# Performance work log

Hardware: AMD Instinct MI355X
Metric: run time of the kernel (lower is better)

The kernel has to match this reference:

```python
import jax, jax.numpy as jnp
import numpy as np

B, S, D, H = 8, 2048, 256, 4
HD = D // H  # 64
EPS = 1e-5


def setup_inputs() -> dict:
    key = jax.random.key(0)
    ks = jax.random.split(key, 16)
    sc = 0.05
    return {
        "descriptors": jax.random.normal(ks[0], (B, S, D), jnp.float32),
        "source": jax.random.normal(ks[1], (B, S, D), jnp.float32),
        "mask": jnp.ones((B, S), jnp.int32),
        # attention projections (stored as [in, out])
        "q_w": jax.random.normal(ks[2], (D, D), jnp.float32) * sc,
        "q_b": jnp.zeros((D,), jnp.float32),
        "k_w": jax.random.normal(ks[3], (D, D), jnp.float32) * sc,
        "k_b": jnp.zeros((D,), jnp.float32),
        "v_w": jax.random.normal(ks[4], (D, D), jnp.float32) * sc,
        "v_b": jnp.zeros((D,), jnp.float32),
        "o_w": jax.random.normal(ks[5], (D, D), jnp.float32) * sc,
        "o_b": jnp.zeros((D,), jnp.float32),
        # MLP layer 0: 2D -> 2D, BatchNorm1d (eval mode) + ReLU
        "m0_w": jax.random.normal(ks[6], (2 * D, 2 * D), jnp.float32) * sc,
        "m0_b": jnp.zeros((2 * D,), jnp.float32),
        "bn_g": jax.random.uniform(ks[7], (2 * D,), jnp.float32, 0.5, 1.5),
        "bn_b": jax.random.normal(ks[8], (2 * D,), jnp.float32) * 0.1,
        "bn_m": jax.random.normal(ks[9], (2 * D,), jnp.float32) * 0.1,
        "bn_v": jax.random.uniform(ks[10], (2 * D,), jnp.float32, 0.5, 1.5),
        # MLP layer 1: 2D -> D, no activation
        "m1_w": jax.random.normal(ks[11], (2 * D, D), jnp.float32) * sc,
        "m1_b": jnp.zeros((D,), jnp.float32),
    }


def reference(descriptors, source, mask, q_w, q_b, k_w, k_b, v_w, v_b, o_w, o_b,
              m0_w, m0_b, bn_g, bn_b, bn_m, bn_v, m1_w, m1_b):
    # Multi-head cross-attention: query=descriptors, key=value=source
    q = (descriptors @ q_w + q_b).reshape(B, S, H, HD).transpose(0, 2, 1, 3)  # [B,H,S,HD]
    k = (source @ k_w + k_b).reshape(B, S, H, HD).transpose(0, 2, 1, 3)
    v = (source @ v_w + v_b).reshape(B, S, H, HD).transpose(0, 2, 1, 3)

    scores = jnp.einsum("bhqd,bhkd->bhqk", q, k) / jnp.sqrt(jnp.float32(HD))
    scores = jnp.where(mask[:, None, None, :] == 0, -1e9, scores)
    probs = jax.nn.softmax(scores.astype(jnp.float32), axis=-1)  # [B,H,S,S]

    ctx = jnp.einsum("bhqk,bhkd->bhqd", probs, v)  # [B,H,S,HD]
    ctx = ctx.transpose(0, 2, 1, 3).reshape(B, S, D)
    attn_out = ctx @ o_w + o_b  # out_proj

    # concat + MLP (Linear -> BatchNorm1d(eval) -> ReLU -> Linear)
    h = jnp.concatenate([descriptors, attn_out], axis=-1)  # [B,S,2D]
    h = h @ m0_w + m0_b
    h = (h - bn_m) * jax.lax.rsqrt(bn_v + EPS) * bn_g + bn_b  # per-channel BN
    h = jax.nn.relu(h)
    h = h @ m1_w + m1_b  # [B,S,D]
    return h
```

## Files before the change

kernel.cpp:

```cpp
#include <hip/hip_runtime.h>

#define NB 8
#define NS 2048
#define ND 256
#define NH 4
#define NHD 64
#define ND2 512
#define NM (NB * NS)
#define C1 0.18033688f

typedef __attribute__((ext_vector_type(8))) short          bf16x8;
typedef __attribute__((ext_vector_type(4))) float          f32x4;
typedef __attribute__((ext_vector_type(16))) float         f32x16;
typedef unsigned short ushort_t;
typedef unsigned int   uint_t;

#define MFMA16(a, b, c) __builtin_amdgcn_mfma_f32_16x16x32_bf16(a, b, c, 0, 0, 0)
#define MFMA32(a, b, c) __builtin_amdgcn_mfma_f32_32x32x16_bf16(a, b, c, 0, 0, 0)

#if __has_builtin(__builtin_amdgcn_exp2f)
#define EXP2(x) __builtin_amdgcn_exp2f(x)
#else
#define EXP2(x) exp2f(x)
#endif

static __device__ inline uint_t pack2bf(float a, float b) {
    union { float f; uint_t u; } x, y; x.f = a; y.f = b;
    return __builtin_amdgcn_perm(y.u + 0x8000u, x.u + 0x8000u, 0x07060302u);
}
static __device__ inline ushort_t f2bf(float f) {
    union { float f; uint_t u; } x; x.f = f;
    return (ushort_t)((x.u + 0x7FFFu + ((x.u >> 16) & 1u)) >> 16);
}
static __device__ inline uint_t cvtpk_bf16(float a, float b) {
    uint_t r;
    asm("v_cvt_pk_bf16_f32 %0, %1, %2" : "=v"(r) : "v"(a), "v"(b));
    return r;
}
static __device__ inline void plswap(uint_t &a, uint_t &b) {
    asm("v_permlane32_swap_b32 %0, %1" : "+v"(a), "+v"(b));
}


static __device__ inline void femit(ushort_t* buf, int n, int k, float v) {
    const int kc = k >> 5;
    const int lane = (((k >> 3) & 3) << 4) | (n & 15);
    const int j = k & 7;
    buf[((size_t)(((n >> 4) * 16 + kc) * 64 + lane)) * 8 + j] = f2bf(v);
}

__global__ __launch_bounds__(256) void prep(
    const float* __restrict__ desc, const float* __restrict__ srcp,
    const int* __restrict__ mask,
    const float* __restrict__ q_w, const float* __restrict__ k_w,
    const float* __restrict__ v_w, const float* __restrict__ m1_w,
    const float* __restrict__ o_w, const float* __restrict__ o_b,
    const float* __restrict__ m0_w, const float* __restrict__ m0_b,
    const float* __restrict__ bng, const float* __restrict__ bnb,
    const float* __restrict__ bnm, const float* __restrict__ bnv,
    ushort_t* __restrict__ descF, ushort_t* __restrict__ srcF,
    ushort_t* __restrict__ qwF, ushort_t* __restrict__ kwF,
    ushort_t* __restrict__ vwF, ushort_t* __restrict__ m1F,
    ushort_t* __restrict__ m0fF, float* __restrict__ biasf,
    uint_t* __restrict__ mbits)
{
    __shared__ float ow[256];
    const int blk = blockIdx.x;
    const int t = threadIdx.x;

    if (blk < 4096) {
        const int y = blk >> 11, x = blk & 2047;
        const float* src = y ? srcp : desc;
        ushort_t* dst    = y ? srcF : descF;
        const int g = x * 256 + t;
        const int lane = g & 63, ci = g >> 6;
        const int kc = ci & 7, r16 = ci >> 3;
        const int row = r16 * 16 + (lane & 15);
        const int c0  = kc * 32 + (lane >> 4) * 8;
        const float* p = src + (size_t)row * ND + c0;
        float4 a = *(const float4*)p;
        float4 b = *(const float4*)(p + 4);
        uint4 pk;
        pk.x = pack2bf(a.x, a.y); pk.y = pack2bf(a.z, a.w);
        pk.z = pack2bf(b.x, b.y); pk.w = pack2bf(b.z, b.w);
        *(uint4*)(dst + (size_t)g * 8) = pk;
    } else if (blk < 4352) {
        const int wb = blk - 4096;
        const int y = wb >> 6, x = wb & 63;
        const float* src; ushort_t* dst; int K, N; float sc = 1.0f;
        switch (y) {
            case 0: src = q_w; dst = qwF; K = 256; N = 256; sc = C1; break;
            case 1: src = k_w; dst = kwF; K = 256; N = 256; break;
            case 2: src = v_w; dst = vwF; K = 256; N = 256; break;
            default: src = m1_w; dst = m1F; K = 512; N = 256; break;
        }
        const int g = x * 256 + t;
        if (g >= (N * K) / 8) return;
        const int lane = g & 63, ci = g >> 6;
        const int lgck = (K == 512) ? 4 : 3;
        const int kc = ci & ((1 << lgck) - 1), n16 = ci >> lgck;
        const int n  = n16 * 16 + (lane & 15);
        const int k0 = kc * 32 + (lane >> 4) * 8;
        float f[8];
#pragma unroll
        for (int j = 0; j < 8; j++) f[j] = src[(size_t)(k0 + j) * N + n] * sc;
        uint4 pk;
        pk.x = pack2bf(f[0], f[1]); pk.y = pack2bf(f[2], f[3]);
        pk.z = pack2bf(f[4], f[5]); pk.w = pack2bf(f[6], f[7]);
        *(uint4*)(dst + (size_t)g * 8) = pk;
    } else if (blk < 4354) {
        const int g = (blk - 4352) * 256 + t;
        const int base = g * 32;
        uint_t m = 0;
#pragma unroll
        for (int j = 0; j < 32; j++) m |= (mask[base + j] ? 1u : 0u) << j;
        mbits[g] = m;
    } else if (blk < 4610) {
        const int i = blk - 4354;
        ow[t] = o_w[i * 256 + t];
        __syncthreads();
        float f0 = 0.f, f1 = 0.f;
#pragma unroll 4
        for (int j = 0; j < 256; j++) {
            const float w = ow[j];
            f0 += w * m0_w[(size_t)(256 + j) * 512 + t];
            f1 += w * m0_w[(size_t)(256 + j) * 512 + t + 256];
        }
        const float A0v = bng[t] * rsqrtf(bnv[t] + 1e-5f);
        const float A1v = bng[t + 256] * rsqrtf(bnv[t + 256] + 1e-5f);
        femit(m0fF, t, 256 + i, f0 * A0v);
        femit(m0fF, t + 256, 256 + i, f1 * A1v);
        femit(m0fF, t, i, m0_w[(size_t)i * 512 + t] * A0v);
        femit(m0fF, t + 256, i, m0_w[(size_t)i * 512 + t + 256] * A1v);
    } else {
        const int bb = blk - 4610;
        const int n  = bb * 32 + (t >> 3);
        const int jp = t & 7;
        float s = 0.f;
#pragma unroll 4
        for (int j = jp * 32; j < jp * 32 + 32; j++)
            s += o_b[j] * m0_w[(size_t)(256 + j) * 512 + n];
        s += __shfl_xor(s, 1);
        s += __shfl_xor(s, 2);
        s += __shfl_xor(s, 4);
        if (jp == 0) {
            const float A = bng[n] * rsqrtf(bnv[n] + 1e-5f);
            biasf[n] = (m0_b[n] + s - bnm[n]) * A + bnb[n];
        }
    }
}

template <int KC, int AK, bool NAT, int MT>
static __device__ inline void core(
    const ushort_t* __restrict__ A0, const ushort_t* __restrict__ A1,
    const ushort_t* __restrict__ WF, int t16, int n16, f32x4 acc[MT][4])
{
    const int lane = threadIdx.x & 63;
#pragma unroll
    for (int kc = 0; kc < KC; kc++) {
        const ushort_t* Ab = (kc < AK) ? A0 : A1;
        const int kca = (kc < AK) ? kc : kc - AK;
        bf16x8 af[MT], wf[4];
#pragma unroll
        for (int mt = 0; mt < MT; mt++)
            af[mt] = *(const bf16x8*)(Ab + ((size_t)((t16 + mt) * AK + kca) * 64 + lane) * 8);
#pragma unroll
        for (int nt = 0; nt < 4; nt++)
            wf[nt] = *(const bf16x8*)(WF + ((size_t)((n16 + nt) * KC + kc) * 64 + lane) * 8);
#pragma unroll
        for (int mt = 0; mt < MT; mt++)
#pragma unroll
            for (int nt = 0; nt < 4; nt++) {
                if (NAT) acc[mt][nt] = MFMA16(af[mt], wf[nt], acc[mt][nt]);
                else     acc[mt][nt] = MFMA16(wf[nt], af[mt], acc[mt][nt]);
            }
    }
}

__global__ __launch_bounds__(256) void qkv_frag(
    const ushort_t* __restrict__ descF, const ushort_t* __restrict__ srcF,
    const ushort_t* __restrict__ qwF, const ushort_t* __restrict__ kwF,
    const ushort_t* __restrict__ vwF,
    const float* __restrict__ q_b, const float* __restrict__ k_b,
    const float* __restrict__ v_b,
    ushort_t* __restrict__ qF, ushort_t* __restrict__ kF,
    ushort_t* __restrict__ vF)
{
    const int t = threadIdx.x, w = t >> 6;
    const int lq = t & 15, lg = (t & 63) >> 4;
    const int h    = blockIdx.x;
    const int tok0 = (blockIdx.y << 7) + (w << 5);
    const int t16  = tok0 >> 4, n16 = h << 2;
    const int z    = blockIdx.z;

    f32x4 acc[2][4];
#pragma unroll
    for (int mt = 0; mt < 2; mt++)
#pragma unroll
        for (int nt = 0; nt < 4; nt++) acc[mt][nt] = (f32x4){0.f, 0.f, 0.f, 0.f};

    if (z == 2) {
        core<8, 8, true, 2>(srcF, srcF, vwF, t16, n16, acc);
#pragma unroll
        for (int nt = 0; nt < 4; nt++) {
            const int dvh = nt * 16 + lq;
            const float bs = v_b[h * 64 + dvh];
#pragma unroll
            for (int mt = 0; mt < 2; mt++) {
                const int tok = tok0 + mt * 16 + lg * 4;
                const int b = tok >> 11, s0 = tok & 2047;
                const int bh = b * NH + h;
                uint2 pv;
                pv.x = pack2bf(acc[mt][nt][0] + bs, acc[mt][nt][1] + bs);
                pv.y = pack2bf(acc[mt][nt][2] + bs, acc[mt][nt][3] + bs);
                const size_t e = (size_t)bh * 131072 +
                    ((size_t)((dvh >> 4) * 64 + (s0 >> 5)) * 64 +
                     (((s0 >> 3) & 3) * 16 + (dvh & 15))) * 8 + (s0 & 7);
                *(uint2*)(vF + e) = pv;
            }
        }
    } else {
        const ushort_t* A = z ? srcF : descF;
        const ushort_t* W = z ? kwF : qwF;
        const float* bias = z ? k_b : q_b;
        ushort_t* dst     = z ? kF : qF;
        const float bsc   = z ? 1.0f : C1;
        core<8, 8, false, 2>(A, A, W, t16, n16, acc);
#pragma unroll
        for (int nt = 0; nt < 4; nt++) {
            const int d0 = nt * 16 + lg * 4;
            f32x4 b4 = *(const f32x4*)(bias + h * 64 + d0);
#pragma unroll
            for (int mt = 0; mt < 2; mt++) {
                const int tok = tok0 + mt * 16 + lq;
                const int b = tok >> 11, s = tok & 2047;
                const int bh = b * NH + h;
                uint2 pv;
                pv.x = pack2bf(acc[mt][nt][0] + b4[0] * bsc,
                               acc[mt][nt][1] + b4[1] * bsc);
                pv.y = pack2bf(acc[mt][nt][2] + b4[2] * bsc,
                               acc[mt][nt][3] + b4[3] * bsc);
                const size_t e = (size_t)bh * 131072 +
                    ((size_t)((s >> 4) * 2 + (d0 >> 5)) * 64 +
                     (((d0 >> 3) & 3) * 16 + lq)) * 8 + (d0 & 7);
                *(uint2*)(dst + e) = pv;
            }
        }
    }
}

__global__ __launch_bounds__(256) void mlp0_frag(
    const ushort_t* __restrict__ descF, const ushort_t* __restrict__ ctxF,
    const ushort_t* __restrict__ m0fF, const float* __restrict__ biasf,
    ushort_t* __restrict__ hF)
{
    const int t = threadIdx.x, w = t >> 6;
    const int lq = t & 15, lg = (t & 63) >> 4;
    const int n0   = blockIdx.x << 6;
    const int tok0 = (blockIdx.y << 7) + (w << 5);
    const int t16  = tok0 >> 4, n16 = n0 >> 4;

    f32x4 acc[2][4];
#pragma unroll
    for (int mt = 0; mt < 2; mt++)
#pragma unroll
        for (int nt = 0; nt < 4; nt++) acc[mt][nt] = (f32x4){0.f, 0.f, 0.f, 0.f};

    core<16, 8, false, 2>(descF, ctxF, m0fF, t16, n16, acc);

#pragma unroll
    for (int nt = 0; nt < 4; nt++) {
        const int c0 = n0 + nt * 16 + lg * 4;
        f32x4 b4 = *(const f32x4*)(biasf + c0);
#pragma unroll
        for (int mt = 0; mt < 2; mt++) {
            const int tok = tok0 + mt * 16 + lq;
            uint2 pv;
            pv.x = pack2bf(fmaxf(acc[mt][nt][0] + b4[0], 0.f),
                           fmaxf(acc[mt][nt][1] + b4[1], 0.f));
            pv.y = pack2bf(fmaxf(acc[mt][nt][2] + b4[2], 0.f),
                           fmaxf(acc[mt][nt][3] + b4[3], 0.f));
            const size_t e = ((size_t)((tok >> 4) * 16 + (c0 >> 5)) * 64 +
                              (((c0 >> 3) & 3) * 16 + lq)) * 8 + (c0 & 7);
            *(uint2*)(hF + e) = pv;
        }
    }
}

__global__ __launch_bounds__(256) void mlp1_frag(
    const ushort_t* __restrict__ hF, const ushort_t* __restrict__ m1F,
    const float* __restrict__ m1_b, float* __restrict__ out)
{
    const int t = threadIdx.x, w = t >> 6;
    const int lq = t & 15, lg = (t & 63) >> 4;
    const int n0   = blockIdx.x << 6;
    const int tok0 = (blockIdx.y << 6) + (w << 4);
    const int t16  = tok0 >> 4, n16 = n0 >> 4;

    f32x4 acc[1][4];
#pragma unroll
    for (int nt = 0; nt < 4; nt++) acc[0][nt] = (f32x4){0.f, 0.f, 0.f, 0.f};

    core<16, 16, false, 1>(hF, hF, m1F, t16, n16, acc);

#pragma unroll
    for (int nt = 0; nt < 4; nt++) {
        const int c0 = n0 + nt * 16 + lg * 4;
        f32x4 b4 = *(const f32x4*)(m1_b + c0);
        const int tok = tok0 + lq;
        f32x4 o4;
#pragma unroll
        for (int j = 0; j < 4; j++) o4[j] = acc[0][nt][j] + b4[j];
        *(f32x4*)(out + (size_t)tok * ND + c0) = o4;
    }
}

__global__ __launch_bounds__(256) void attn_frag(
    const ushort_t* __restrict__ qF, const ushort_t* __restrict__ kF,
    const ushort_t* __restrict__ vF, const uint_t* __restrict__ mbits,
    ushort_t* __restrict__ ctxF)
{
    __shared__ f32x4 Ob[2][2][4][64];
    __shared__ float Ls[2][64];

    const int t = threadIdx.x, w = t >> 6, lane = t & 63;
    const int wq = w & 1, kw = w >> 1;
    const int q = lane & 31, h = lane >> 5;
    const int flat = blockIdx.x + (blockIdx.y << 5) + (blockIdx.z << 7);
    const int bh = (flat & 7) + (((flat >> 8) & 3) << 3);
    const int qb = (flat >> 3) & 31;

    const ushort_t* qh = qF + (size_t)bh * 131072;
    const ushort_t* kh = kF + (size_t)bh * 131072;
    const ushort_t* vh = vF + (size_t)bh * 131072;
    const uint_t* mw = mbits + (bh >> 2) * 64 + (kw << 5);

    const int qrow0 = qb * 64 + wq * 32;
    const int tok = qrow0 + q;
    const int kbase = kw << 10;

    bf16x8 qf[4];
#pragma unroll
    for (int st = 0; st < 4; st++)
        qf[st] = *(const bf16x8*)(qh +
            ((size_t)(((tok >> 4) * 2 + (st >> 1)) * 64 +
                      ((st * 2 + h) & 3) * 16 + (tok & 15))) * 8);

    f32x16 o[2];
#pragma unroll
    for (int dt = 0; dt < 2; dt++)
#pragma unroll
        for (int j = 0; j < 16; j++) o[dt][j] = 0.f;
    float l_part = 0.0f;

    bf16x8 ka[2][4];
#pragma unroll
    for (int kt = 0; kt < 2; kt++)
#pragma unroll
        for (int st = 0; st < 4; st++) {
            const int key = kbase + kt * 32 + q;
            ka[kt][st] = *(const bf16x8*)(kh +
                ((size_t)(((key >> 4) * 2 + (st >> 1)) * 64 +
                          ((st * 2 + h) & 3) * 16 + (key & 15))) * 8);
        }

    for (int k0 = 0; k0 < 1024; k0 += 64) {
        const int key0 = kbase + k0;

        bf16x8 vf[2][4];
#pragma unroll
        for (int dt = 0; dt < 2; dt++)
#pragma unroll
            for (int st = 0; st < 4; st++) {
                const int d = dt * 32 + q;
                vf[dt][st] = *(const bf16x8*)(vh +
                    ((size_t)(((d >> 4) * 64 + (key0 >> 5) + (st >> 1)) * 64 +
                              ((st * 2 + h) & 3) * 16 + (d & 15))) * 8);
            }

        const uint_t mw0 = mw[(k0 >> 5)];
        const uint_t mw1 = mw[(k0 >> 5) + 1];

        f32x16 sa[2];
#pragma unroll
        for (int kt = 0; kt < 2; kt++)
#pragma unroll
            for (int j = 0; j < 16; j++) sa[kt][j] = 0.f;

        __builtin_amdgcn_s_setprio(1);
#pragma unroll
        for (int kt = 0; kt < 2; kt++)
#pragma unroll
            for (int st = 0; st < 4; st++)
                sa[kt] = MFMA32(ka[kt][st], qf[st], sa[kt]);
        __builtin_amdgcn_s_setprio(0);

        const int keyn = kbase + ((k0 + 64) & 1023);
#pragma unroll
        for (int kt = 0; kt < 2; kt++)
#pragma unroll
            for (int st = 0; st < 4; st++) {
                const int key = keyn + kt * 32 + q;
                ka[kt][st] = *(const bf16x8*)(kh +
                    ((size_t)(((key >> 4) * 2 + (st >> 1)) * 64 +
                              ((st * 2 + h) & 3) * 16 + (key & 15))) * 8);
            }

        float ls0 = 0.f, ls1 = 0.f, ls2 = 0.f, ls3 = 0.f;
        uint_t W[2][4][2];

#define SMAX_BODY(DM)                                                         \
        _Pragma("unroll")                                                     \
        for (int kt = 0; kt < 2; kt++) {                                      \
            _Pragma("unroll")                                                 \
            for (int r1 = 0; r1 < 4; r1++) {                                  \
                _Pragma("unroll")                                             \
                for (int wv = 0; wv < 2; wv++) {                              \
                    float p0 = EXP2(sa[kt][r1 * 4 + wv * 2]);                 \
                    float p1 = EXP2(sa[kt][r1 * 4 + wv * 2 + 1]);             \
                    if (DM) {                                                 \
                        const uint_t mk = (kt ? mw1 : mw0) >> (h * 4);        \
                        if (!((mk >> (r1 * 8 + wv * 2)) & 1u)) p0 = 0.f;      \
                        if (!((mk >> (r1 * 8 + wv * 2)) & 2u)) p1 = 0.f;      \
                    }                                                         \
                    if (kt == 0) { if (wv == 0) ls0 += p0 + p1;               \
                                   else         ls1 += p0 + p1; }             \
                    else         { if (wv == 0) ls2 += p0 + p1;               \
                                   else         ls3 += p0 + p1; }             \
                    W[kt][r1][wv] = cvtpk_bf16(p0, p1);                       \
                }                                                             \
            }                                                                 \
        }

        if (__builtin_expect((mw0 & mw1) != 0xFFFFFFFFu, 0)) {
            SMAX_BODY(1)
        } else {
            SMAX_BODY(0)
        }
#undef SMAX_BODY
        l_part += (ls0 + ls1) + (ls2 + ls3);

#pragma unroll
        for (int kt = 0; kt < 2; kt++)
#pragma unroll
            for (int s1 = 0; s1 < 2; s1++)
#pragma unroll
                for (int wv = 0; wv < 2; wv++)
                    plswap(W[kt][2 * s1][wv], W[kt][2 * s1 + 1][wv]);

        __builtin_amdgcn_s_setprio(1);
#pragma unroll
        for (int st = 0; st < 4; st++) {
            const int kt = st >> 1, s1 = st & 1;
            union { uint_t u[4]; bf16x8 v; } pb;
            pb.u[0] = W[kt][2 * s1][0];
            pb.u[1] = W[kt][2 * s1][1];
            pb.u[2] = W[kt][2 * s1 + 1][0];
            pb.u[3] = W[kt][2 * s1 + 1][1];
#pragma unroll
            for (int dt = 0; dt < 2; dt++)
                o[dt] = MFMA32(vf[dt][st], pb.v, o[dt]);
        }
        __builtin_amdgcn_s_setprio(0);
    }

    l_part += __shfl_xor(l_part, 32);

    if (kw) {
#pragma unroll
        for (int dt = 0; dt < 2; dt++)
#pragma unroll
            for (int r1 = 0; r1 < 4; r1++) {
                f32x4 v;
#pragma unroll
                for (int r0 = 0; r0 < 4; r0++) v[r0] = o[dt][r1 * 4 + r0];
                Ob[wq][dt][r1][lane] = v;
            }
        Ls[wq][lane] = l_part;
    }
    __syncthreads();
    if (kw) return;

    const float li = 1.0f / (l_part + Ls[wq][lane]);

    const int tok16 = (bh >> 2) * 128 + (tok >> 4);
#pragma unroll
    for (int dt = 0; dt < 2; dt++)
#pragma unroll
        for (int r1 = 0; r1 < 4; r1++) {
            const f32x4 p = Ob[wq][dt][r1][lane];
            const int c = (bh & 3) * 64 + dt * 32 + r1 * 8 + h * 4;
            uint2 pv;
            pv.x = cvtpk_bf16((o[dt][r1 * 4 + 0] + p[0]) * li,
                              (o[dt][r1 * 4 + 1] + p[1]) * li);
            pv.y = cvtpk_bf16((o[dt][r1 * 4 + 2] + p[2]) * li,
                              (o[dt][r1 * 4 + 3] + p[3]) * li);
            const size_t e = ((size_t)(tok16 * 8 + (c >> 5)) * 64 +
                              (((c >> 3) & 3) * 16 + (tok & 15))) * 8 + (c & 7);
            *(uint2*)(ctxF + e) = pv;
        }
}

extern "C" void kernel_launch(void* const* d_in, const int* in_sizes, int n_in,
                              void* d_out, int out_size, void* d_ws, size_t ws_size,
                              hipStream_t stream)
{
    (void)in_sizes; (void)n_in; (void)out_size; (void)ws_size;
    const float* desc = (const float*)d_in[0];
    const float* srcp = (const float*)d_in[1];
    const int*   mask = (const int*)d_in[2];
    const float* q_w  = (const float*)d_in[3];
    const float* q_b  = (const float*)d_in[4];
    const float* k_w  = (const float*)d_in[5];
    const float* k_b  = (const float*)d_in[6];
    const float* v_w  = (const float*)d_in[7];
    const float* v_b  = (const float*)d_in[8];
    const float* o_w  = (const float*)d_in[9];
    const float* o_b  = (const float*)d_in[10];
    const float* m0_w = (const float*)d_in[11];
    const float* m0_b = (const float*)d_in[12];
    const float* bng  = (const float*)d_in[13];
    const float* bnb  = (const float*)d_in[14];
    const float* bnm  = (const float*)d_in[15];
    const float* bnv  = (const float*)d_in[16];
    const float* m1_w = (const float*)d_in[17];
    const float* m1_b = (const float*)d_in[18];
    float* out = (float*)d_out;

    const size_t ASZ = (size_t)NM * ND;
    ushort_t* descF = (ushort_t*)d_ws;
    ushort_t* srcF  = descF + ASZ;
    ushort_t* qF    = descF + 2 * ASZ;
    ushort_t* kF    = descF + 3 * ASZ;
    ushort_t* vF    = descF + 4 * ASZ;
    ushort_t* qwF   = descF + 5 * ASZ;
    ushort_t* kwF   = qwF + 65536;
    ushort_t* vwF   = kwF + 65536;
    ushort_t* m1F   = vwF + 65536;
    ushort_t* m0fF  = m1F + 131072;
    float*    biasf = (float*)(m0fF + 262144);
    uint_t*   mbits = (uint_t*)(biasf + 512);
    ushort_t* ctxF  = srcF;
    ushort_t* hF    = qF;

    const dim3 blk(256);

    prep<<<dim3(4626), blk, 0, stream>>>(
        desc, srcp, mask, q_w, k_w, v_w, m1_w, o_w, o_b, m0_w, m0_b,
        bng, bnb, bnm, bnv, descF, srcF, qwF, kwF, vwF, m1F, m0fF, biasf, mbits);

    qkv_frag<<<dim3(4, NM / 128, 3), blk, 0, stream>>>(
        descF, srcF, qwF, kwF, vwF, q_b, k_b, v_b, qF, kF, vF);
    attn_frag<<<dim3(NS / 64, NH, NB), blk, 0, stream>>>(qF, kF, vF, mbits, ctxF);
    mlp0_frag<<<dim3(8, NM / 128), blk, 0, stream>>>(descF, ctxF, m0fF, biasf, hF);
    mlp1_frag<<<dim3(4, NM / 64), blk, 0, stream>>>(hF, m1F, m1_b, out);
}
```

Measured before the change: 241.1 us.

## Double-buffer GEMM fragment loads and remap blocks for XCD-aware L2 locality

Restructures the shared GEMM inner loop to prefetch the next k-chunk's A and W fragments into a second register set while MFMAs run on the current set, hiding global load latency. The projection and MLP kernels also switch to a flat 1D grid with a remapped block index, so consecutive blocks on the same XCD (F&7) work on neighbouring token tiles and share the same weight/activation tiles in L2. This costs more live registers and some index arithmetic per block.

```diff
diff --git a/kernel.cpp b/kernel.cpp
--- a/kernel.cpp
+++ b/kernel.cpp
@@ -151,30 +151,51 @@
 }
 
 template <int KC, int AK, bool NAT, int MT>
-static __device__ inline void core(
+static __device__ inline void core_db(
     const ushort_t* __restrict__ A0, const ushort_t* __restrict__ A1,
     const ushort_t* __restrict__ WF, int t16, int n16, f32x4 acc[MT][4])
 {
     const int lane = threadIdx.x & 63;
-#pragma unroll
-    for (int kc = 0; kc < KC; kc++) {
-        const ushort_t* Ab = (kc < AK) ? A0 : A1;
-        const int kca = (kc < AK) ? kc : kc - AK;
-        bf16x8 af[MT], wf[4];
-#pragma unroll
-        for (int mt = 0; mt < MT; mt++)
-            af[mt] = *(const bf16x8*)(Ab + ((size_t)((t16 + mt) * AK + kca) * 64 + lane) * 8);
-#pragma unroll
-        for (int nt = 0; nt < 4; nt++)
-            wf[nt] = *(const bf16x8*)(WF + ((size_t)((n16 + nt) * KC + kc) * 64 + lane) * 8);
-#pragma unroll
-        for (int mt = 0; mt < MT; mt++)
-#pragma unroll
-            for (int nt = 0; nt < 4; nt++) {
-                if (NAT) acc[mt][nt] = MFMA16(af[mt], wf[nt], acc[mt][nt]);
-                else     acc[mt][nt] = MFMA16(wf[nt], af[mt], acc[mt][nt]);
-            }
-    }
+
+#define LDA(KCI, AF)                                                          \
+    {                                                                         \
+        const ushort_t* Ab = ((KCI) < AK) ? A0 : A1;                          \
+        const int kca = ((KCI) < AK) ? (KCI) : (KCI) - AK;                    \
+        _Pragma("unroll")                                                     \
+        for (int mt = 0; mt < MT; mt++)                                       \
+            AF[mt] = *(const bf16x8*)(Ab +                                    \
+                ((size_t)((t16 + mt) * AK + kca) * 64 + lane) * 8);           \
+    }
+#define LDW(KCI, WFR)                                                         \
+    {                                                                         \
+        _Pragma("unroll")                                                     \
+        for (int nt = 0; nt < 4; nt++)                                        \
+            WFR[nt] = *(const bf16x8*)(WF +                                   \
+                ((size_t)((n16 + nt) * KC + (KCI)) * 64 + lane) * 8);         \
+    }
+#define DOMFMA(AF, WFR)                                                       \
+    {                                                                         \
+        _Pragma("unroll")                                                     \
+        for (int mt = 0; mt < MT; mt++)                                       \
+            _Pragma("unroll")                                                 \
+            for (int nt = 0; nt < 4; nt++) {                                  \
+                if (NAT) acc[mt][nt] = MFMA16(AF[mt], WFR[nt], acc[mt][nt]);  \
+                else     acc[mt][nt] = MFMA16(WFR[nt], AF[mt], acc[mt][nt]);  \
+            }                                                                 \
+    }
+
+    bf16x8 afA[MT], wfA[4], afB[MT], wfB[4];
+    LDA(0, afA); LDW(0, wfA);
+#pragma unroll
+    for (int kc = 0; kc < KC; kc += 2) {
+        if (kc + 1 < KC) { LDA(kc + 1, afB); LDW(kc + 1, wfB); }
+        DOMFMA(afA, wfA);
+        if (kc + 2 < KC) { LDA(kc + 2, afA); LDW(kc + 2, wfA); }
+        if (kc + 1 < KC) DOMFMA(afB, wfB);
+    }
+#undef LDA
+#undef LDW
+#undef DOMFMA
 }
 
 __global__ __launch_bounds__(256) void qkv_frag(
@@ -188,10 +209,14 @@
 {
     const int t = threadIdx.x, w = t >> 6;
     const int lq = t & 15, lg = (t & 63) >> 4;
-    const int h    = blockIdx.x;
-    const int tok0 = (blockIdx.y << 7) + (w << 5);
+    const int F = blockIdx.x;
+    const int L = (F & 7) * 192 + (F >> 3);
+    const int m = L % 192;
+    const int yy = m / 12, r = m % 12;
+    const int h = r & 3, z = r >> 2;
+    const int y = (L / 192) * 16 + yy;
+    const int tok0 = (y << 7) + (w << 5);
     const int t16  = tok0 >> 4, n16 = h << 2;
-    const int z    = blockIdx.z;
 
     f32x4 acc[2][4];
 #pragma unroll
@@ -200,7 +225,7 @@
         for (int nt = 0; nt < 4; nt++) acc[mt][nt] = (f32x4){0.f, 0.f, 0.f, 0.f};
 
     if (z == 2) {
-        core<8, 8, true, 2>(srcF, srcF, vwF, t16, n16, acc);
+        core_db<8, 8, true, 2>(srcF, srcF, vwF, t16, n16, acc);
 #pragma unroll
         for (int nt = 0; nt < 4; nt++) {
             const int dvh = nt * 16 + lq;
@@ -225,7 +250,7 @@
         const float* bias = z ? k_b : q_b;
         ushort_t* dst     = z ? kF : qF;
         const float bsc   = z ? 1.0f : C1;
-        core<8, 8, false, 2>(A, A, W, t16, n16, acc);
+        core_db<8, 8, false, 2>(A, A, W, t16, n16, acc);
 #pragma unroll
         for (int nt = 0; nt < 4; nt++) {
             const int d0 = nt * 16 + lg * 4;
@@ -256,8 +281,13 @@
 {
     const int t = threadIdx.x, w = t >> 6;
     const int lq = t & 15, lg = (t & 63) >> 4;
-    const int n0   = blockIdx.x << 6;
-    const int tok0 = (blockIdx.y << 7) + (w << 5);
+    const int F = blockIdx.x;
+    const int L = (F & 7) * 128 + (F >> 3);
+    const int m = L % 128;
+    const int yy = m >> 3, nx = m & 7;
+    const int y = (L / 128) * 16 + yy;
+    const int n0   = nx << 6;
+    const int tok0 = (y << 7) + (w << 5);
     const int t16  = tok0 >> 4, n16 = n0 >> 4;
 
     f32x4 acc[2][4];
@@ -266,7 +296,7 @@
 #pragma unroll
         for (int nt = 0; nt < 4; nt++) acc[mt][nt] = (f32x4){0.f, 0.f, 0.f, 0.f};
 
-    core<16, 8, false, 2>(descF, ctxF, m0fF, t16, n16, acc);
+    core_db<16, 8, false, 2>(descF, ctxF, m0fF, t16, n16, acc);
 
 #pragma unroll
     for (int nt = 0; nt < 4; nt++) {
@@ -293,15 +323,20 @@
 {
     const int t = threadIdx.x, w = t >> 6;
     const int lq = t & 15, lg = (t & 63) >> 4;
-    const int n0   = blockIdx.x << 6;
-    const int tok0 = (blockIdx.y << 6) + (w << 4);
+    const int F = blockIdx.x;
+    const int L = (F & 7) * 128 + (F >> 3);
+    const int m = L % 128;
+    const int yy = m >> 2, nx = m & 3;
+    const int y = (L / 128) * 32 + yy;
+    const int n0   = nx << 6;
+    const int tok0 = (y << 6) + (w << 4);
     const int t16  = tok0 >> 4, n16 = n0 >> 4;
 
     f32x4 acc[1][4];
 #pragma unroll
     for (int nt = 0; nt < 4; nt++) acc[0][nt] = (f32x4){0.f, 0.f, 0.f, 0.f};
 
-    core<16, 16, false, 1>(hF, hF, m1F, t16, n16, acc);
+    core_db<16, 16, false, 1>(hF, hF, m1F, t16, n16, acc);
 
 #pragma unroll
     for (int nt = 0; nt < 4; nt++) {
@@ -549,9 +584,9 @@
         desc, srcp, mask, q_w, k_w, v_w, m1_w, o_w, o_b, m0_w, m0_b,
         bng, bnb, bnm, bnv, descF, srcF, qwF, kwF, vwF, m1F, m0fF, biasf, mbits);
 
-    qkv_frag<<<dim3(4, NM / 128, 3), blk, 0, stream>>>(
+    qkv_frag<<<dim3(1536), blk, 0, stream>>>(
         descF, srcF, qwF, kwF, vwF, q_b, k_b, v_b, qF, kF, vF);
     attn_frag<<<dim3(NS / 64, NH, NB), blk, 0, stream>>>(qF, kF, vF, mbits, ctxF);
-    mlp0_frag<<<dim3(8, NM / 128), blk, 0, stream>>>(descF, ctxF, m0fF, biasf, hF);
-    mlp1_frag<<<dim3(4, NM / 64), blk, 0, stream>>>(hF, m1F, m1_b, out);
-}
+    mlp0_frag<<<dim3(1024), blk, 0, stream>>>(descF, ctxF, m0fF, biasf, hF);
+    mlp1_frag<<<dim3(1024), blk, 0, stream>>>(hF, m1F, m1_b, out);
+}
```

Result: faster. 230.1 us (-4.6%).
